# Performance work log

Measured on AMD Instinct MI355X. Metric: run time of the kernel, lower is better.

The kernel has to match this reference:

```python
import jax, jax.numpy as jnp
import numpy as np

B, N, E, D = 4, 2048, 2048, 2048  # batch, seq, embedding_dim, out_dim


def setup_inputs() -> dict:
    key = jax.random.key(0)
    k1, k2, k3 = jax.random.split(key, 3)
    x = jax.random.normal(k1, (B, N, E), dtype=jnp.float32)
    # qkv_proj: Linear(E, 3*D). Store weight as [E, 3D] for x @ W.
    W = jax.random.normal(k2, (E, 3 * D), dtype=jnp.float32) * (1.0 / np.sqrt(E))
    b = jax.random.normal(k3, (3 * D,), dtype=jnp.float32) * 0.01
    return {"x": x, "W": W, "b": b}


def reference(x, W, b):
    d = W.shape[1] // 3
    n = x.shape[1]
    qkv = x @ W + b                                   # [B, N, 3D]
    q, k, v = jnp.split(qkv, 3, axis=-1)              # each [B, N, D]
    scale = 1.0 / np.sqrt(d).astype(np.float32)
    att = jnp.einsum('bqd,bkd->bqk', q, k) * scale    # [B, N, N]
    causal = jnp.tril(jnp.ones((n, n), dtype=bool))
    att = jnp.where(causal[None, :, :], att, -jnp.inf)
    # softmax_with_denom: stable softmax, also return the denominator
    m = jnp.max(att, axis=-1, keepdims=True)
    e = jnp.exp(att - m)
    denom = jnp.sum(e, axis=-1)                       # [B, N]
    p = e / denom[..., None]
    y = jnp.einsum('bqk,bkd->bqd', p, v)              # [B, N, D]
    return y, denom
```

## Files before the change

### kernel.cpp

```cpp
#include <hip/hip_runtime.h>

typedef unsigned short u16;
typedef unsigned int   u32;

#define SEQ 2048
#define EMB 2048
#define TD  6144

using bf16x8 = __attribute__((ext_vector_type(8))) __bf16;
using f32x4  = __attribute__((ext_vector_type(4))) float;

typedef __attribute__((address_space(1))) const void* gas_t;
typedef __attribute__((address_space(3))) void*       las_t;
#define GLOAD16(g, l) __builtin_amdgcn_global_load_lds((gas_t)(g), (las_t)(l), 16, 0, 0)

__device__ __forceinline__ u16 f2bf(float f) {
  u32 u = __float_as_uint(f);
  u += 0x7fffu + ((u >> 16) & 1u);
  return (u16)(u >> 16);
}

__global__ __launch_bounds__(256) void cast_x_kern(const float* __restrict__ x,
                                                   u16* __restrict__ xb) {
  size_t i = ((size_t)blockIdx.x * 256 + threadIdx.x) * 4;
  float4 v = *(const float4*)(x + i);
  ushort4 u;
  u.x = f2bf(v.x); u.y = f2bf(v.y); u.z = f2bf(v.z); u.w = f2bf(v.w);
  *(ushort4*)(xb + i) = u;
}

__global__ __launch_bounds__(256) void castT_W_kern(const float* __restrict__ W,
                                                    u16* __restrict__ Wt) {
  __shared__ float t[64][65];
  int c0 = blockIdx.x * 64, r0 = blockIdx.y * 64;
  int tid = threadIdx.x;
#pragma unroll
  for (int i = 0; i < 4; ++i) {
    int flat = i * 1024 + tid * 4;
    int r = flat >> 6, c = flat & 63;
    float4 v = *(const float4*)(W + (size_t)(r0 + r) * TD + c0 + c);
    t[r][c] = v.x; t[r][c + 1] = v.y; t[r][c + 2] = v.z; t[r][c + 3] = v.w;
  }
  __syncthreads();
#pragma unroll
  for (int i = 0; i < 4; ++i) {
    int flat = i * 1024 + tid * 4;
    int wr = flat >> 6, wc = flat & 63;
    ushort4 u;
    u.x = f2bf(t[wc + 0][wr]); u.y = f2bf(t[wc + 1][wr]);
    u.z = f2bf(t[wc + 2][wr]); u.w = f2bf(t[wc + 3][wr]);
    *(ushort4*)(Wt + (size_t)(c0 + wr) * EMB + r0 + wc) = u;
  }
}

__global__ __launch_bounds__(256) void transpose_v_kern(const u16* __restrict__ qkv,
                                                        u16* __restrict__ vT) {
  __shared__ u16 t[64][68];
  int b = blockIdx.z;
  int d0 = blockIdx.x * 64, n0 = blockIdx.y * 64;
  const u16* src = qkv + (size_t)b * SEQ * TD + 2 * SEQ;
  u16* dst = vT + (size_t)b * SEQ * SEQ;
  int tid = threadIdx.x;
#pragma unroll
  for (int i = 0; i < 4; ++i) {
    int flat = i * 1024 + tid * 4;
    int n = flat >> 6, d = flat & 63;
    *(ushort4*)&t[n][d] = *(const ushort4*)(src + (size_t)(n0 + n) * TD + d0 + d);
  }
  __syncthreads();
#pragma unroll
  for (int i = 0; i < 4; ++i) {
    int flat = i * 1024 + tid * 4;
    int d = flat >> 6, n = flat & 63;
    ushort4 u;
    u.x = t[n + 0][d]; u.y = t[n + 1][d]; u.z = t[n + 2][d]; u.w = t[n + 3][d];
    *(ushort4*)(dst + (size_t)(d0 + d) * SEQ + n0 + n) = u;
  }
}

template <int MODE>
__global__ __launch_bounds__(512, 2) void gemm256(const u16* __restrict__ Ab,
                                                  const u16* __restrict__ Bb,
                                                  void* __restrict__ Cb,
                                                  const float* __restrict__ bias) {
  __shared__ u16 sA0[16384];
  __shared__ u16 sB0[16384];
  __shared__ u16 sA1[16384];
  __shared__ u16 sB1[16384];

  constexpr int lda = (MODE == 0) ? EMB : (MODE == 1) ? TD : 4096;
  constexpr int ldb = (MODE == 0) ? EMB : (MODE == 1) ? TD : SEQ;
  constexpr int NWG = (MODE == 0) ? 768 : (MODE == 1) ? 144 : 256;
  constexpr int CPX = NWG / 8;

  int bid = blockIdx.x;
  int wg = (bid & 7) * CPX + (bid >> 3);

  const u16 *A, *Bt;
  int row0, col0, nk;
  size_t coff = 0;
  if constexpr (MODE == 0) {
    A = Ab; Bt = Bb;
    row0 = (wg / 24) * 256; col0 = (wg % 24) * 256; nk = EMB / 64;
  } else if constexpr (MODE == 1) {
    int b = wg / 36, tq = wg % 36;
    int qi = (int)((sqrtf(8.f * (float)tq + 1.f) - 1.f) * 0.5f);
    while ((qi + 1) * (qi + 2) / 2 <= tq) ++qi;
    while (qi * (qi + 1) / 2 > tq) --qi;
    int kj = tq - qi * (qi + 1) / 2;
    A = Ab + (size_t)b * SEQ * TD;
    Bt = A + EMB;
    row0 = qi * 256; col0 = kj * 256; nk = EMB / 64;
    coff = (size_t)b * SEQ * SEQ;
  } else {
    int b = wg >> 6, qi = (wg >> 3) & 7, nj = wg & 7;
    A = Ab + (size_t)b * SEQ * 4096;
    Bt = Bb + (size_t)b * SEQ * SEQ;
    row0 = qi * 256; col0 = nj * 256; nk = (qi + 1) * 4;
    coff = (size_t)b * SEQ * SEQ;
  }

  int tid = threadIdx.x;
  int wave = tid >> 6, lane = tid & 63;
  int wm = wave >> 2, wn = wave & 3;
  int ln = lane & 15;

  auto stageB = [&](auto& SB, int i, int t) {
    int ob = i * 8192 + wave * 1024;
    int obl = ob + lane * 16;
    int row = obl >> 7, cb = obl & 127;
    int c = ((cb ^ ((row & 7) << 4)) >> 1) + t * 64;
    GLOAD16(Bt + (size_t)(col0 + row) * ldb + c, (char*)SB + ob);
  };
  auto stageA = [&](auto& SA, int i, int t) {
    int ob = i * 4096 + ((wave < 4) ? wave * 1024 : 16384 + (wave - 4) * 1024);
    int obl = ob + lane * 16;
    int row = obl >> 7, cb = obl & 127;
    int c = ((cb ^ ((row & 7) << 4)) >> 1) + t * 64;
    GLOAD16(A + (size_t)(row0 + row) * lda + c, (char*)SA + ob);
  };

  auto ldfrag = [&](auto& S, int rr, int ks) -> bf16x8 {
    int cb = ks * 64 + (lane >> 4) * 16;
    return *(const bf16x8*)((const char*)S + rr * 128 + (cb ^ ((rr & 7) << 4)));
  };

  f32x4 acc[8][4];
#pragma unroll
  for (int m = 0; m < 8; ++m)
#pragma unroll
    for (int n = 0; n < 4; ++n) acc[m][n] = (f32x4){0.f, 0.f, 0.f, 0.f};

  auto tile_step = [&](auto& CA, auto& CB, auto& NA, auto& NB, int t) {
    bool pf = (t + 1 < nk);
    bf16x8 bfg[4][2], afg[2][2];
#pragma unroll
    for (int n = 0; n < 4; ++n)
#pragma unroll
      for (int ks = 0; ks < 2; ++ks)
        bfg[n][ks] = ldfrag(CB, wn * 64 + n * 16 + ln, ks);
#pragma unroll
    for (int m = 0; m < 2; ++m)
#pragma unroll
      for (int ks = 0; ks < 2; ++ks)
        afg[m][ks] = ldfrag(CA, wm * 128 + m * 16 + ln, ks);
    if (pf) { stageB(NB, 0, t + 1); stageB(NB, 1, t + 1);
              stageA(NA, 0, t + 1); stageA(NA, 1, t + 1); }
    asm volatile("s_waitcnt lgkmcnt(8)" ::: "memory");
    __builtin_amdgcn_s_barrier();
    asm volatile("s_waitcnt lgkmcnt(0)" ::: "memory");
    __builtin_amdgcn_s_setprio(1);
#pragma unroll
    for (int m = 0; m < 2; ++m)
#pragma unroll
      for (int n = 0; n < 4; ++n)
#pragma unroll
        for (int ks = 0; ks < 2; ++ks)
          acc[m][n] = __builtin_amdgcn_mfma_f32_16x16x32_bf16(
              afg[m][ks], bfg[n][ks], acc[m][n], 0, 0, 0);
    __builtin_amdgcn_s_setprio(0);
#pragma unroll
    for (int p = 1; p < 4; ++p) {
#pragma unroll
      for (int m = 0; m < 2; ++m)
#pragma unroll
        for (int ks = 0; ks < 2; ++ks)
          afg[m][ks] = ldfrag(CA, wm * 128 + p * 32 + m * 16 + ln, ks);
      if (p == 1 && pf) { stageB(NB, 2, t + 1); stageB(NB, 3, t + 1);
                          stageA(NA, 2, t + 1); stageA(NA, 3, t + 1); }
      __builtin_amdgcn_s_barrier();
      asm volatile("s_waitcnt lgkmcnt(0)" ::: "memory");
      __builtin_amdgcn_s_setprio(1);
#pragma unroll
      for (int m = 0; m < 2; ++m)
#pragma unroll
        for (int n = 0; n < 4; ++n)
#pragma unroll
          for (int ks = 0; ks < 2; ++ks)
            acc[p * 2 + m][n] = __builtin_amdgcn_mfma_f32_16x16x32_bf16(
                afg[m][ks], bfg[n][ks], acc[p * 2 + m][n], 0, 0, 0);
      __builtin_amdgcn_s_setprio(0);
      if (p == 3) {
        asm volatile("s_waitcnt vmcnt(0)" ::: "memory");
        __builtin_amdgcn_s_barrier();
      }
    }
  };

#pragma unroll
  for (int bi = 0; bi < 4; ++bi) stageB(sB0, bi, 0);
#pragma unroll
  for (int bi = 0; bi < 4; ++bi) stageA(sA0, bi, 0);
  asm volatile("s_waitcnt vmcnt(0)" ::: "memory");
  __builtin_amdgcn_s_barrier();

  for (int t2 = 0; t2 < nk; t2 += 2) {
    tile_step(sA0, sB0, sA1, sB1, t2);
    tile_step(sA1, sB1, sA0, sB0, t2 + 1);
  }

  int l4 = (lane >> 4) << 2;
  int rb = row0 + wm * 128, cb0 = col0 + wn * 64;
  if constexpr (MODE == 0) {
    u16* C = (u16*)Cb;
#pragma unroll
    for (int n = 0; n < 4; ++n) {
      float bv = bias[cb0 + n * 16 + ln];
#pragma unroll
      for (int m = 0; m < 8; ++m)
#pragma unroll
        for (int r = 0; r < 4; ++r)
          C[(size_t)(rb + m * 16 + l4 + r) * TD + cb0 + n * 16 + ln] =
              f2bf(acc[m][n][r] + bv);
    }
  } else if constexpr (MODE == 1) {
    float* C = (float*)Cb + coff;
    const float scale = 0.022097086912079608f;
#pragma unroll
    for (int m = 0; m < 8; ++m)
#pragma unroll
      for (int n = 0; n < 4; ++n)
#pragma unroll
        for (int r = 0; r < 4; ++r)
          C[(size_t)(rb + m * 16 + l4 + r) * SEQ + cb0 + n * 16 + ln] =
              acc[m][n][r] * scale;
  } else {
    float* C = (float*)Cb + coff;
#pragma unroll
    for (int m = 0; m < 8; ++m)
#pragma unroll
      for (int n = 0; n < 4; ++n)
#pragma unroll
        for (int r = 0; r < 4; ++r)
          C[(size_t)(rb + m * 16 + l4 + r) * SEQ + cb0 + n * 16 + ln] = acc[m][n][r];
  }
}

__global__ __launch_bounds__(256) void softmax_kern(const float* __restrict__ att,
                                                    u16* __restrict__ P,
                                                    float* __restrict__ denom) {
  int row = blockIdx.x;
  int q = row & (SEQ - 1);
  const float* arow = att + (size_t)row * SEQ;
  u16* prow = P + (size_t)row * 4096;
  int jlen = ((q >> 8) + 1) << 8;
  int tid = threadIdx.x;
  int j0 = tid * 4, j1 = tid * 4 + 1024;
  float NI = -__builtin_inff();
  float4 a0 = make_float4(NI, NI, NI, NI), a1 = a0;
  if (j0 < jlen) a0 = *(const float4*)(arow + j0);
  if (j1 < jlen) a1 = *(const float4*)(arow + j1);
  if (j0 + 0 > q) a0.x = NI;
  if (j0 + 1 > q) a0.y = NI;
  if (j0 + 2 > q) a0.z = NI;
  if (j0 + 3 > q) a0.w = NI;
  if (j1 + 0 > q) a1.x = NI;
  if (j1 + 1 > q) a1.y = NI;
  if (j1 + 2 > q) a1.z = NI;
  if (j1 + 3 > q) a1.w = NI;
  float mx = fmaxf(fmaxf(fmaxf(a0.x, a0.y), fmaxf(a0.z, a0.w)),
                   fmaxf(fmaxf(a1.x, a1.y), fmaxf(a1.z, a1.w)));
#pragma unroll
  for (int off = 32; off; off >>= 1) mx = fmaxf(mx, __shfl_xor(mx, off, 64));
  __shared__ float red[8];
  int wv = tid >> 6;
  if ((tid & 63) == 0) red[wv] = mx;
  __syncthreads();
  mx = fmaxf(fmaxf(red[0], red[1]), fmaxf(red[2], red[3]));
  a0.x = expf(a0.x - mx); a0.y = expf(a0.y - mx);
  a0.z = expf(a0.z - mx); a0.w = expf(a0.w - mx);
  a1.x = expf(a1.x - mx); a1.y = expf(a1.y - mx);
  a1.z = expf(a1.z - mx); a1.w = expf(a1.w - mx);
  float s = (a0.x + a0.y + a0.z + a0.w) + (a1.x + a1.y + a1.z + a1.w);
#pragma unroll
  for (int off = 32; off; off >>= 1) s += __shfl_xor(s, off, 64);
  if ((tid & 63) == 0) red[4 + wv] = s;
  __syncthreads();
  s = red[4] + red[5] + red[6] + red[7];
  float inv = 1.0f / s;
  if (j0 < jlen) {
    ushort4 u;
    u.x = f2bf(a0.x * inv); u.y = f2bf(a0.y * inv);
    u.z = f2bf(a0.z * inv); u.w = f2bf(a0.w * inv);
    *(ushort4*)(prow + j0) = u;
  }
  if (j1 < jlen) {
    ushort4 u;
    u.x = f2bf(a1.x * inv); u.y = f2bf(a1.y * inv);
    u.z = f2bf(a1.z * inv); u.w = f2bf(a1.w * inv);
    *(ushort4*)(prow + j1) = u;
  }
  if (tid == 0) denom[row] = s;
}

extern "C" void kernel_launch(void* const* d_in, const int* in_sizes, int n_in,
                              void* d_out, int out_size, void* d_ws, size_t ws_size,
                              hipStream_t stream) {
  const float* x    = (const float*)d_in[0];
  const float* W    = (const float*)d_in[1];
  const float* bias = (const float*)d_in[2];

  if (ws_size < 201326592u) return;

  char* w = (char*)d_ws;
  u16*   qkv = (u16*)w;
  u16*   xb  = (u16*)(w + 100663296);
  u16*   Wt  = (u16*)(w + 134217728);
  u16*   vT  = (u16*)(w + 100663296);
  float* att = (float*)(w + 134217728);
  u16*   P   = (u16*)(w + 134217728);

  float* y     = (float*)d_out;
  float* denom = y + (size_t)4 * SEQ * SEQ;

  cast_x_kern<<<16384, 256, 0, stream>>>(x, xb);
  castT_W_kern<<<dim3(96, 32), 256, 0, stream>>>(W, Wt);
  gemm256<0><<<768, 512, 0, stream>>>(xb, Wt, qkv, bias);
  transpose_v_kern<<<dim3(32, 32, 4), 256, 0, stream>>>(qkv, vT);
  gemm256<1><<<144, 512, 0, stream>>>(qkv, nullptr, att, nullptr);
  softmax_kern<<<8192, 256, 0, stream>>>(att, P, denom);
  gemm256<2><<<256, 512, 0, stream>>>(P, vT, y, nullptr);
}
```

Before: 365.8 us.

## Software-pipeline LDS fragment loads across quarters and tiles in GEMM mainloop

Restructures the GEMM inner loop so each quarter's A fragments and the next tile's B/A fragments are loaded from LDS while the previous quarter's MFMAs run, using ping-pong register sets and double-buffered B fragments. All global-to-LDS prefetches for the next tile are issued at the start of the step instead of being split across two phases. The aim is to hide LDS read latency behind MFMA work and cut barrier stalls. In exchange it uses more registers for the extra fragment buffers, which can lower occupancy, and it relies on hand-tuned waitcnt values that must be exactly right to stay correct.

```diff
diff --git a/kernel.cpp b/kernel.cpp
--- a/kernel.cpp
+++ b/kernel.cpp
@@ -13,6 +13,8 @@
 typedef __attribute__((address_space(1))) const void* gas_t;
 typedef __attribute__((address_space(3))) void*       las_t;
 #define GLOAD16(g, l) __builtin_amdgcn_global_load_lds((gas_t)(g), (las_t)(l), 16, 0, 0)
+
+template <int N> struct IC { static constexpr int value = N; };
 
 __device__ __forceinline__ u16 f2bf(float f) {
   u32 u = __float_as_uint(f);
@@ -125,22 +127,21 @@
   int wm = wave >> 2, wn = wave & 3;
   int ln = lane & 15;
 
-  auto stageB = [&](auto& SB, int i, int t) {
+  auto stageB = [&](u16* SB, int i, int t) {
     int ob = i * 8192 + wave * 1024;
     int obl = ob + lane * 16;
     int row = obl >> 7, cb = obl & 127;
     int c = ((cb ^ ((row & 7) << 4)) >> 1) + t * 64;
     GLOAD16(Bt + (size_t)(col0 + row) * ldb + c, (char*)SB + ob);
   };
-  auto stageA = [&](auto& SA, int i, int t) {
+  auto stageA = [&](u16* SA, int i, int t) {
     int ob = i * 4096 + ((wave < 4) ? wave * 1024 : 16384 + (wave - 4) * 1024);
     int obl = ob + lane * 16;
     int row = obl >> 7, cb = obl & 127;
     int c = ((cb ^ ((row & 7) << 4)) >> 1) + t * 64;
     GLOAD16(A + (size_t)(row0 + row) * lda + c, (char*)SA + ob);
   };
-
-  auto ldfrag = [&](auto& S, int rr, int ks) -> bf16x8 {
+  auto ldfrag = [&](const u16* S, int rr, int ks) -> bf16x8 {
     int cb = ks * 64 + (lane >> 4) * 16;
     return *(const bf16x8*)((const char*)S + rr * 128 + (cb ^ ((rr & 7) << 4)));
   };
@@ -151,60 +152,70 @@
 #pragma unroll
     for (int n = 0; n < 4; ++n) acc[m][n] = (f32x4){0.f, 0.f, 0.f, 0.f};
 
-  auto tile_step = [&](auto& CA, auto& CB, auto& NA, auto& NB, int t) {
+  bf16x8 aP[2][2], aQ[2][2];
+  bf16x8 bR[2][4][2];
+
+  auto LOADQ = [&](bf16x8 (&dst)[2][2], const u16* S, int q) {
+#pragma unroll
+    for (int m = 0; m < 2; ++m)
+#pragma unroll
+      for (int ks = 0; ks < 2; ++ks)
+        dst[m][ks] = ldfrag(S, wm * 128 + q * 32 + m * 16 + ln, ks);
+  };
+  auto LOADB = [&](bf16x8 (&dst)[4][2], const u16* S) {
+#pragma unroll
+    for (int n = 0; n < 4; ++n)
+#pragma unroll
+      for (int ks = 0; ks < 2; ++ks)
+        dst[n][ks] = ldfrag(S, wn * 64 + n * 16 + ln, ks);
+  };
+  auto MFMAQ = [&](auto QC, bf16x8 (&Af)[2][2], bf16x8 (&Bf)[4][2]) {
+    constexpr int q = decltype(QC)::value;
+    __builtin_amdgcn_s_setprio(1);
+#pragma unroll
+    for (int m = 0; m < 2; ++m)
+#pragma unroll
+      for (int n = 0; n < 4; ++n)
+#pragma unroll
+        for (int ks = 0; ks < 2; ++ks)
+          acc[q * 2 + m][n] = __builtin_amdgcn_mfma_f32_16x16x32_bf16(
+              Af[m][ks], Bf[n][ks], acc[q * 2 + m][n], 0, 0, 0);
+    __builtin_amdgcn_s_setprio(0);
+  };
+
+  auto tile_step = [&](const u16* CA, const u16* CB, u16* NA, u16* NB, int t, auto TPC) {
+    constexpr int tp = decltype(TPC)::value;
     bool pf = (t + 1 < nk);
-    bf16x8 bfg[4][2], afg[2][2];
-#pragma unroll
-    for (int n = 0; n < 4; ++n)
-#pragma unroll
-      for (int ks = 0; ks < 2; ++ks)
-        bfg[n][ks] = ldfrag(CB, wn * 64 + n * 16 + ln, ks);
-#pragma unroll
-    for (int m = 0; m < 2; ++m)
-#pragma unroll
-      for (int ks = 0; ks < 2; ++ks)
-        afg[m][ks] = ldfrag(CA, wm * 128 + m * 16 + ln, ks);
-    if (pf) { stageB(NB, 0, t + 1); stageB(NB, 1, t + 1);
-              stageA(NA, 0, t + 1); stageA(NA, 1, t + 1); }
-    asm volatile("s_waitcnt lgkmcnt(8)" ::: "memory");
+    LOADQ(aQ, CA, 1);
+    if (pf) {
+      stageB(NB, 0, t + 1); stageB(NB, 1, t + 1); stageB(NB, 2, t + 1); stageB(NB, 3, t + 1);
+      stageA(NA, 0, t + 1); stageA(NA, 1, t + 1); stageA(NA, 2, t + 1); stageA(NA, 3, t + 1);
+    }
+    asm volatile("s_waitcnt lgkmcnt(4)" ::: "memory");
+    __builtin_amdgcn_sched_barrier(0);
+    MFMAQ(IC<0>{}, aP, bR[tp]);
     __builtin_amdgcn_s_barrier();
-    asm volatile("s_waitcnt lgkmcnt(0)" ::: "memory");
-    __builtin_amdgcn_s_setprio(1);
-#pragma unroll
-    for (int m = 0; m < 2; ++m)
-#pragma unroll
-      for (int n = 0; n < 4; ++n)
-#pragma unroll
-        for (int ks = 0; ks < 2; ++ks)
-          acc[m][n] = __builtin_amdgcn_mfma_f32_16x16x32_bf16(
-              afg[m][ks], bfg[n][ks], acc[m][n], 0, 0, 0);
-    __builtin_amdgcn_s_setprio(0);
-#pragma unroll
-    for (int p = 1; p < 4; ++p) {
-#pragma unroll
-      for (int m = 0; m < 2; ++m)
-#pragma unroll
-        for (int ks = 0; ks < 2; ++ks)
-          afg[m][ks] = ldfrag(CA, wm * 128 + p * 32 + m * 16 + ln, ks);
-      if (p == 1 && pf) { stageB(NB, 2, t + 1); stageB(NB, 3, t + 1);
-                          stageA(NA, 2, t + 1); stageA(NA, 3, t + 1); }
-      __builtin_amdgcn_s_barrier();
+    LOADQ(aP, CA, 2);
+    asm volatile("s_waitcnt lgkmcnt(4)" ::: "memory");
+    __builtin_amdgcn_sched_barrier(0);
+    MFMAQ(IC<1>{}, aQ, bR[tp]);
+    __builtin_amdgcn_s_barrier();
+    LOADQ(aQ, CA, 3);
+    asm volatile("s_waitcnt lgkmcnt(4)" ::: "memory");
+    __builtin_amdgcn_sched_barrier(0);
+    MFMAQ(IC<2>{}, aP, bR[tp]);
+    if (pf) asm volatile("s_waitcnt vmcnt(0)" ::: "memory");
+    __builtin_amdgcn_s_barrier();
+    if (pf) {
+      LOADQ(aP, NA, 0);
+      LOADB(bR[tp ^ 1], NB);
+      asm volatile("s_waitcnt lgkmcnt(12)" ::: "memory");
+    } else {
       asm volatile("s_waitcnt lgkmcnt(0)" ::: "memory");
-      __builtin_amdgcn_s_setprio(1);
-#pragma unroll
-      for (int m = 0; m < 2; ++m)
-#pragma unroll
-        for (int n = 0; n < 4; ++n)
-#pragma unroll
-          for (int ks = 0; ks < 2; ++ks)
-            acc[p * 2 + m][n] = __builtin_amdgcn_mfma_f32_16x16x32_bf16(
-                afg[m][ks], bfg[n][ks], acc[p * 2 + m][n], 0, 0, 0);
-      __builtin_amdgcn_s_setprio(0);
-      if (p == 3) {
-        asm volatile("s_waitcnt vmcnt(0)" ::: "memory");
-        __builtin_amdgcn_s_barrier();
-      }
     }
+    __builtin_amdgcn_sched_barrier(0);
+    MFMAQ(IC<3>{}, aQ, bR[tp]);
+    __builtin_amdgcn_s_barrier();
   };
 
 #pragma unroll
@@ -213,10 +224,12 @@
   for (int bi = 0; bi < 4; ++bi) stageA(sA0, bi, 0);
   asm volatile("s_waitcnt vmcnt(0)" ::: "memory");
   __builtin_amdgcn_s_barrier();
+  LOADQ(aP, sA0, 0);
+  LOADB(bR[0], sB0);
 
   for (int t2 = 0; t2 < nk; t2 += 2) {
-    tile_step(sA0, sB0, sA1, sB1, t2);
-    tile_step(sA1, sB1, sA0, sB0, t2 + 1);
+    tile_step(sA0, sB0, sA1, sB1, t2,     IC<0>{});
+    tile_step(sA1, sB1, sA0, sB0, t2 + 1, IC<1>{});
   }
 
   int l4 = (lane >> 4) << 2;
```

New measurement: 554.5 us. 51.6% more time.
